# Kernel optimization log

Measured on AMD Instinct MI355X. Metric: run time of the kernel, lower is better.

Reference implementation:

```python
import jax, jax.numpy as jnp
import numpy as np

EMBED_DIM = 256
MIN_SCALE = 0.5
BASE = 100.0
NDIM = 3
EPS = 1e-5


def basis_norm(psi, w):
    # w: [B, N] float weights; reduce over token dim (-2)
    norm_sq = jnp.sum(w[..., None] * (psi * psi), axis=-2, keepdims=True)
    return psi / jnp.sqrt(norm_sq + EPS)


def rotary(f, coords, lift):
    # lift: [D//2, 3]; phase: [B, N, D//2]
    phase = coords @ lift.T
    c, s = jnp.cos(phase), jnp.sin(phase)
    f1, f2 = jnp.split(f, 2, axis=-1)
    return jnp.concatenate([f1 * c - f2 * s, f1 * s + f2 * c], axis=-1)


def setup_inputs() -> dict:
    key = jax.random.key(0)
    ks = jax.random.split(key, 12)
    B, N, D = 4, 8192, EMBED_DIM
    phi = jax.random.normal(ks[0], (B, N, D), dtype=jnp.float32)
    coords = jax.random.normal(ks[1], (B, N, NDIM), dtype=jnp.float32)
    weights = jax.random.uniform(ks[2], (B, N), dtype=jnp.float32)
    scale = 1.0 / np.sqrt(D)
    Wq = jax.random.normal(ks[3], (D, D), dtype=jnp.float32) * scale
    bq = jnp.zeros((D,), dtype=jnp.float32)
    Wk = jax.random.normal(ks[4], (D, D), dtype=jnp.float32) * scale
    bk = jax.random.normal(ks[5], (D,), dtype=jnp.float32) * 0.01
    Wv = jax.random.normal(ks[6], (D, D), dtype=jnp.float32) * scale
    bv = jax.random.normal(ks[7], (D,), dtype=jnp.float32) * 0.01
    Wo = jax.random.normal(ks[8], (D, D), dtype=jnp.float32) * scale
    bo = jnp.zeros((D,), dtype=jnp.float32)
    # rotary lift init: k_norms * random unit vecs
    half = D // 2
    scales = BASE ** (-2.0 * np.arange(half) / D)
    k_norms = (2.0 * np.pi / MIN_SCALE) * scales  # [half]
    u = np.asarray(jax.random.normal(ks[9], (half, NDIM)))
    u = u / np.linalg.norm(u, axis=-1, keepdims=True)
    lift = jnp.asarray(k_norms[:, None] * u, dtype=jnp.float32)  # [half, 3]
    return {"phi": phi, "coords": coords, "weights": weights,
            "Wq": Wq, "bq": bq, "Wk": Wk, "bk": bk, "Wv": Wv, "bv": bv,
            "Wo": Wo, "bo": bo, "lift": lift}


def reference(phi, coords, weights, Wq, bq, Wk, bk, Wv, bv, Wo, bo, lift):
    q = phi @ Wq.T + bq
    k = basis_norm(phi @ Wk.T + bk, weights)
    v = basis_norm(phi @ Wv.T + bv, weights)
    q = rotary(q, coords, lift)
    k = rotary(k, coords, lift)
    k = k * weights[..., None]  # float-weights branch
    kv = jnp.einsum('bnd,bne->bde', k, v)   # [B, D, D]
    out = jnp.einsum('bnd,bde->bne', q, kv)  # [B, N, D]
    return out @ Wo.T + bo
```

## Files before the change

### kernel.cpp

```cpp
#include <hip/hip_runtime.h>
#include <hip/hip_bf16.h>
#include <stdint.h>

#define DEV __device__ __forceinline__

typedef short short8 __attribute__((ext_vector_type(8)));
typedef float floatx4 __attribute__((ext_vector_type(4)));

constexpr int D = 256;
constexpr int NTOK = 8192;
constexpr int MTOT = 4 * NTOK;

DEV void gl_lds16(const void* g, void* l) {
  __builtin_amdgcn_global_load_lds(
      (const __attribute__((address_space(1))) void*)g,
      (__attribute__((address_space(3))) void*)l, 16, 0, 0);
}

DEV float bflo(uint32_t u) { return __uint_as_float(u << 16); }
DEV float bfhi(uint32_t u) { return __uint_as_float(u & 0xffff0000u); }
DEV uint32_t packbf(float a, float b) {
  uint16_t xa = __builtin_bit_cast(uint16_t, __float2bfloat16(a));
  uint16_t xb = __builtin_bit_cast(uint16_t, __float2bfloat16(b));
  return (uint32_t)xa | ((uint32_t)xb << 16);
}

constexpr int PHI_E = MTOT * D;
constexpr int W_E = D * D;

__global__ __launch_bounds__(256) void convert(
    const float* __restrict__ phi, const float* __restrict__ Wq,
    const float* __restrict__ Wk, const float* __restrict__ Wv,
    const float* __restrict__ Wo,
    uint2* __restrict__ dst, float2* __restrict__ nszero) {
  if (blockIdx.x == 0) {
    const float2 z = {0.f, 0.f};
#pragma unroll
    for (int k = 0; k < 4; k++) nszero[k * 256 + threadIdx.x] = z;
  }
  const int idx4 = blockIdx.x * 256 + threadIdx.x;
  const int e0 = idx4 * 4;
  float4 v;
  if (e0 < PHI_E) {
    v = ((const float4*)phi)[idx4];
  } else {
    const int r = e0 - PHI_E;
    const int m = r >> 16;
    const int q = (r & 65535) >> 2;
    const float4* src = (m == 0) ? (const float4*)Wq : (m == 1) ? (const float4*)Wk
                      : (m == 2) ? (const float4*)Wv : (const float4*)Wo;
    v = src[q];
  }
  uint2 o;
  o.x = packbf(v.x, v.y);
  o.y = packbf(v.z, v.w);
  dst[idx4] = o;
}

__global__ __launch_bounds__(256, 4) void gemm_qkv(
    const __hip_bfloat16* __restrict__ phi,
    const __hip_bfloat16* __restrict__ W16,
    const float* __restrict__ bq, const float* __restrict__ bk, const float* __restrict__ bv,
    const float* __restrict__ coords, const float* __restrict__ wts,
    const float* __restrict__ lift,
    __hip_bfloat16* __restrict__ Qb, __hip_bfloat16* __restrict__ Kb,
    __hip_bfloat16* __restrict__ Vb, float* __restrict__ nsk, float* __restrict__ nsv) {
  __shared__ __align__(16) char As[8192];
  __shared__ __align__(16) char Bs[8192];
  const int t = threadIdx.x, lane = t & 63, wid = t >> 6;
  const int wm = (wid & 1) * 64;
  const int wn = (wid >> 1) * 32;
  const int l16 = lane & 15, q4 = lane >> 4;
  const int bid = blockIdx.x;
  const int g = (bid & 7) * 192 + (bid >> 3);
  const int sub = g % 6;
  const int mat = sub >> 1;
  const int nc0 = (sub & 1) * 64;
  const int m0 = (g / 6) * 128;
  const __hip_bfloat16* W = W16 + (size_t)mat * W_E;
  const float* bias = (mat == 0) ? bq : (mat == 1) ? bk : bv;
  __hip_bfloat16* Out = (mat == 0) ? Qb : (mat == 1) ? Kb : Vb;

  floatx4 acc[4][4] = {};

  const int srow = wid * 16 + (lane >> 2);
  const int skoff = (lane & 3) * 8;
  const __hip_bfloat16* gA = phi + (size_t)(m0 + srow) * D + skoff;
  const __hip_bfloat16* gB = W + (size_t)(nc0 + srow) * D + skoff;
  char* lA = As + srow * 64 + skoff * 2;
  char* lB = Bs + srow * 64 + skoff * 2;

  for (int kt = 0; kt < 256; kt += 32) {
    gl_lds16(gA + kt, lA);
    gl_lds16(gA + kt + 64 * D, lA + 4096);
    gl_lds16(gB + kt, lB);
    gl_lds16(gB + kt + 128 * D, lB + 4096);
    __syncthreads();
    short8 af[4], bf4[4];
#pragma unroll
    for (int i = 0; i < 4; i++)
      af[i] = *(const short8*)(As + (wm + i * 16 + l16) * 64 + q4 * 16);
#pragma unroll
    for (int j = 0; j < 4; j++) {
      const int brow = (j >> 1) * 64 + wn + (j & 1) * 16 + l16;
      bf4[j] = *(const short8*)(Bs + brow * 64 + q4 * 16);
    }
#pragma unroll
    for (int i = 0; i < 4; i++)
#pragma unroll
      for (int j = 0; j < 4; j++)
        acc[i][j] = __builtin_amdgcn_mfma_f32_16x16x32_bf16(af[i], bf4[j], acc[i][j], 0, 0, 0);
    __syncthreads();
  }

  float bcol[4];
#pragma unroll
  for (int j = 0; j < 4; j++)
    bcol[j] = bias[nc0 + wn + (j & 1) * 16 + (j >> 1) * 128 + l16];

  if (mat == 0) {
    float lx[2], ly[2], lz[2];
#pragma unroll
    for (int jj = 0; jj < 2; jj++) {
      const int c = nc0 + wn + jj * 16 + l16;
      lx[jj] = lift[c * 3 + 0]; ly[jj] = lift[c * 3 + 1]; lz[jj] = lift[c * 3 + 2];
    }
#pragma unroll
    for (int i = 0; i < 4; i++) {
#pragma unroll
      for (int r = 0; r < 4; r++) {
        const int row = m0 + wm + i * 16 + q4 * 4 + r;
        const float cx = coords[row * 3 + 0];
        const float cy = coords[row * 3 + 1];
        const float cz = coords[row * 3 + 2];
#pragma unroll
        for (int jj = 0; jj < 2; jj++) {
          const int c = nc0 + wn + jj * 16 + l16;
          const float p = cx * lx[jj] + cy * ly[jj] + cz * lz[jj];
          float s, cs;
          __sincosf(p, &s, &cs);
          const float f1 = acc[i][jj][r] + bcol[jj];
          const float f2 = acc[i][jj + 2][r] + bcol[jj + 2];
          Out[(size_t)row * D + c]       = __float2bfloat16(f1 * cs - f2 * s);
          Out[(size_t)row * D + c + 128] = __float2bfloat16(f1 * s + f2 * cs);
        }
      }
    }
  } else {
    const int b = m0 >> 13;
    float* ns = (mat == 1) ? nsk : nsv;
    float colsum[4] = {};
#pragma unroll
    for (int i = 0; i < 4; i++) {
#pragma unroll
      for (int r = 0; r < 4; r++) {
        const int row = m0 + wm + i * 16 + q4 * 4 + r;
        const float w = wts[row];
#pragma unroll
        for (int j = 0; j < 4; j++) {
          const int col = nc0 + wn + (j & 1) * 16 + (j >> 1) * 128 + l16;
          const float psi = acc[i][j][r] + bcol[j];
          Out[(size_t)row * D + col] = __float2bfloat16(psi);
          colsum[j] += w * psi * psi;
        }
      }
    }
#pragma unroll
    for (int j = 0; j < 4; j++) {
      float s = colsum[j];
      s += __shfl_xor(s, 16);
      s += __shfl_xor(s, 32);
      if (q4 == 0) {
        const int col = nc0 + wn + (j & 1) * 16 + (j >> 1) * 128 + l16;
        atomicAdd(&ns[b * D + col], s);
      }
    }
  }
}

__global__ __launch_bounds__(256) void kpoint(
    __hip_bfloat16* __restrict__ Kb, const float* __restrict__ coords,
    const float* __restrict__ wts, const float* __restrict__ lift,
    const float* __restrict__ nsk) {
  const int t = threadIdx.x;
  const int j = t & 63, rloc = t >> 6;
  const int r0 = blockIdx.x * 32;
  const int b = r0 >> 13;
  const int j0 = 2 * j, j1 = 2 * j + 1;
  const float lx0 = lift[j0 * 3 + 0], ly0 = lift[j0 * 3 + 1], lz0 = lift[j0 * 3 + 2];
  const float lx1 = lift[j1 * 3 + 0], ly1 = lift[j1 * 3 + 1], lz1 = lift[j1 * 3 + 2];
  const int nb = b * D;
  const float ik0 = rsqrtf(nsk[nb + j0] + 1e-5f);
  const float ik1 = rsqrtf(nsk[nb + j1] + 1e-5f);
  const float ik2 = rsqrtf(nsk[nb + 128 + j0] + 1e-5f);
  const float ik3 = rsqrtf(nsk[nb + 128 + j1] + 1e-5f);
  uint32_t* K32 = (uint32_t*)Kb;
#pragma unroll
  for (int it = 0; it < 8; it++) {
    const size_t row = (size_t)r0 + it * 4 + rloc;
    const float cx = coords[row * 3 + 0];
    const float cy = coords[row * 3 + 1];
    const float cz = coords[row * 3 + 2];
    const float p0 = cx * lx0 + cy * ly0 + cz * lz0;
    const float p1 = cx * lx1 + cy * ly1 + cz * lz1;
    float s0, c0, s1, c1;
    __sincosf(p0, &s0, &c0);
    __sincosf(p1, &s1, &c1);
    const float w = wts[row];
    const size_t base = row * 128;
    const uint32_t klo = K32[base + j], khi = K32[base + 64 + j];
    const float k1a = bflo(klo) * ik0, k1b = bfhi(klo) * ik1;
    const float k2a = bflo(khi) * ik2, k2b = bfhi(khi) * ik3;
    K32[base + j]      = packbf((k1a * c0 - k2a * s0) * w, (k1b * c1 - k2b * s1) * w);
    K32[base + 64 + j] = packbf((k1a * s0 + k2a * c0) * w, (k1b * s1 + k2b * c1) * w);
  }
}

__global__ __launch_bounds__(256, 2) void gemm_tn(
    const __hip_bfloat16* __restrict__ Kwb, const __hip_bfloat16* __restrict__ Vb,
    __hip_bfloat16* __restrict__ part) {
  __shared__ __align__(16) char Asm[128 * 80];
  __shared__ __align__(16) char Bsm[128 * 80];
  const int t = threadIdx.x, lane = t & 63, wid = t >> 6;
  const int wm = (wid & 1) * 64, wn = (wid >> 1) * 64;
  const int l16 = lane & 15, q4 = lane >> 4;
  const int bid = blockIdx.x;
  const int g = (bid & 7) * 64 + (bid >> 3);
  const int ed = g & 3, rest = g >> 2;
  const int chunk = rest & 31, b = rest >> 5;
  const int d0 = (ed >> 1) * 128, e0 = (ed & 1) * 128;
  const uint32_t* A32 = (const uint32_t*)Kwb;
  const uint32_t* B32 = (const uint32_t*)Vb;
  const int s_np = (((t & 3) | ((t >> 6) << 2)) ^ ((t >> 4) & 3));
  const int s_e2lo = (t >> 2) & 15;
  floatx4 acc[4][4] = {};
  for (int nt = 0; nt < 256; nt += 32) {
    const int nbase = chunk * 256 + nt;
    const size_t tokbase = ((size_t)b * NTOK + nbase + 2 * s_np) * 128;
#pragma unroll
    for (int r = 0; r < 4; r++) {
      const int e2 = s_e2lo + r * 16;
      {
        const uint32_t a0 = A32[tokbase + (d0 >> 1) + e2];
        const uint32_t a1 = A32[tokbase + 128 + (d0 >> 1) + e2];
        *(uint32_t*)(Asm + (2 * e2) * 80 + 4 * s_np)     = (a0 & 0xffffu) | (a1 << 16);
        *(uint32_t*)(Asm + (2 * e2 + 1) * 80 + 4 * s_np) = (a0 >> 16) | (a1 & 0xffff0000u);
      }
      {
        const uint32_t b0 = B32[tokbase + (e0 >> 1) + e2];
        const uint32_t b1 = B32[tokbase + 128 + (e0 >> 1) + e2];
        *(uint32_t*)(Bsm + (2 * e2) * 80 + 4 * s_np)     = (b0 & 0xffffu) | (b1 << 16);
        *(uint32_t*)(Bsm + (2 * e2 + 1) * 80 + 4 * s_np) = (b0 >> 16) | (b1 & 0xffff0000u);
      }
    }
    __syncthreads();
    short8 af[4], bf8[4];
#pragma unroll
    for (int i = 0; i < 4; i++) {
      af[i]  = *(const short8*)(Asm + (wm + i * 16 + l16) * 80 + q4 * 16);
      bf8[i] = *(const short8*)(Bsm + (wn + i * 16 + l16) * 80 + q4 * 16);
    }
#pragma unroll
    for (int i = 0; i < 4; i++)
#pragma unroll
      for (int j = 0; j < 4; j++)
        acc[i][j] = __builtin_amdgcn_mfma_f32_16x16x32_bf16(af[i], bf8[j], acc[i][j], 0, 0, 0);
    __syncthreads();
  }
  __hip_bfloat16* pt = part + (((size_t)(chunk * 4 + b)) << 16);
#pragma unroll
  for (int i = 0; i < 4; i++) {
#pragma unroll
    for (int r = 0; r < 4; r++) {
      const int rg = d0 + wm + i * 16 + q4 * 4 + r;
#pragma unroll
      for (int j = 0; j < 4; j++) {
        const int cg = e0 + wn + j * 16 + l16;
        pt[rg * 256 + cg] = __float2bfloat16(acc[i][j][r]);
      }
    }
  }
}

__global__ __launch_bounds__(256) void reduce_kvt(const uint32_t* __restrict__ part,
                                                  uint32_t* __restrict__ Ps,
                                                  const float* __restrict__ nsv) {
  const int flat2 = blockIdx.x * 256 + threadIdx.x;
  const int b = flat2 >> 15;
  const int off = flat2 & 32767;
  const int es = (off & 127) * 2;
  float sx = 0, sy = 0;
#pragma unroll
  for (int c = 0; c < 32; c++) {
    const uint32_t u = part[(((size_t)(c * 4 + b)) << 15) + off];
    sx += bflo(u); sy += bfhi(u);
  }
  const float iv0 = rsqrtf(nsv[b * D + es] + 1e-5f);
  const float iv1 = rsqrtf(nsv[b * D + es + 1] + 1e-5f);
  Ps[flat2] = packbf(sx * iv0, sy * iv1);
}

__global__ __launch_bounds__(256, 4) void gemm_mt(
    const __hip_bfloat16* __restrict__ Wo16, const __hip_bfloat16* __restrict__ Ps,
    __hip_bfloat16* __restrict__ MT) {
  __shared__ __align__(16) char As[8192];
  __shared__ __align__(16) char Bs[8192];
  const int t = threadIdx.x, lane = t & 63, wid = t >> 6;
  const int wm = (wid & 1) * 64, wn = (wid >> 1) * 64;
  const int l16 = lane & 15, q4 = lane >> 4;
  const int m0 = blockIdx.x * 128, n0 = blockIdx.y * 128, b = blockIdx.z;
  const __hip_bfloat16* Bm = Ps + ((size_t)b << 16);
  floatx4 acc[4][4] = {};
  const int srow = wid * 16 + (lane >> 2);
  const int skoff = (lane & 3) * 8;
  const __hip_bfloat16* gA = Wo16 + (size_t)(m0 + srow) * D + skoff;
  const __hip_bfloat16* gB = Bm + (size_t)(n0 + srow) * D + skoff;
  char* lA = As + srow * 64 + skoff * 2;
  char* lB = Bs + srow * 64 + skoff * 2;
  for (int kt = 0; kt < 256; kt += 32) {
    gl_lds16(gA + kt, lA);
    gl_lds16(gA + kt + 64 * D, lA + 4096);
    gl_lds16(gB + kt, lB);
    gl_lds16(gB + kt + 64 * D, lB + 4096);
    __syncthreads();
    short8 af[4], bf8[4];
#pragma unroll
    for (int i = 0; i < 4; i++) {
      af[i]  = *(const short8*)(As + (wm + i * 16 + l16) * 64 + q4 * 16);
      bf8[i] = *(const short8*)(Bs + (wn + i * 16 + l16) * 64 + q4 * 16);
    }
#pragma unroll
    for (int i = 0; i < 4; i++)
#pragma unroll
      for (int j = 0; j < 4; j++)
        acc[i][j] = __builtin_amdgcn_mfma_f32_16x16x32_bf16(af[i], bf8[j], acc[i][j], 0, 0, 0);
    __syncthreads();
  }
  __hip_bfloat16* Ob = MT + ((size_t)b << 16);
#pragma unroll
  for (int j = 0; j < 4; j++) {
    const int colg = n0 + wn + j * 16 + l16;
#pragma unroll
    for (int i = 0; i < 4; i++) {
      const int rowg = m0 + wm + i * 16 + q4 * 4;
#pragma unroll
      for (int r = 0; r < 4; r++)
        Ob[(size_t)(rowg + r) * D + colg] = __float2bfloat16(acc[i][j][r]);
    }
  }
}

__global__ __launch_bounds__(256, 4) void gemm_out(
    const __hip_bfloat16* __restrict__ A, const __hip_bfloat16* __restrict__ Pm,
    const float* __restrict__ bo, float* __restrict__ Og) {
  __shared__ __align__(16) char As[8192];
  __shared__ __align__(16) char Bs[8192];
  const int t = threadIdx.x, lane = t & 63, wid = t >> 6;
  const int wm = (wid & 1) * 64, wn = (wid >> 1) * 64;
  const int l16 = lane & 15, q4 = lane >> 4;
  const int m0 = blockIdx.x * 128, n0 = blockIdx.y * 128;
  const int b = m0 >> 13;
  const __hip_bfloat16* W = Pm + ((size_t)b << 16);
  floatx4 acc[4][4] = {};
  const int srow = wid * 16 + (lane >> 2);
  const int skoff = (lane & 3) * 8;
  const __hip_bfloat16* gA = A + (size_t)(m0 + srow) * D + skoff;
  const __hip_bfloat16* gB = W + (size_t)(n0 + srow) * D + skoff;
  char* lA = As + srow * 64 + skoff * 2;
  char* lB = Bs + srow * 64 + skoff * 2;
  for (int kt = 0; kt < 256; kt += 32) {
    gl_lds16(gA + kt, lA);
    gl_lds16(gA + kt + 64 * D, lA + 4096);
    gl_lds16(gB + kt, lB);
    gl_lds16(gB + kt + 64 * D, lB + 4096);
    __syncthreads();
    short8 af[4], bf8[4];
#pragma unroll
    for (int i = 0; i < 4; i++) {
      af[i]  = *(const short8*)(As + (wm + i * 16 + l16) * 64 + q4 * 16);
      bf8[i] = *(const short8*)(Bs + (wn + i * 16 + l16) * 64 + q4 * 16);
    }
#pragma unroll
    for (int i = 0; i < 4; i++)
#pragma unroll
      for (int j = 0; j < 4; j++)
        acc[i][j] = __builtin_amdgcn_mfma_f32_16x16x32_bf16(af[i], bf8[j], acc[i][j], 0, 0, 0);
    __syncthreads();
  }
#pragma unroll
  for (int j = 0; j < 4; j++) {
    const int colg = n0 + wn + j * 16 + l16;
    const float bb = bo[colg];
#pragma unroll
    for (int i = 0; i < 4; i++) {
      const int rowg = m0 + wm + i * 16 + q4 * 4;
#pragma unroll
      for (int r = 0; r < 4; r++)
        Og[(size_t)(rowg + r) * D + colg] = acc[i][j][r] + bb;
    }
  }
}

extern "C" void kernel_launch(void* const* d_in, const int* in_sizes, int n_in,
                              void* d_out, int out_size, void* d_ws, size_t ws_size,
                              hipStream_t stream) {
  const float* phi    = (const float*)d_in[0];
  const float* coords = (const float*)d_in[1];
  const float* wts    = (const float*)d_in[2];
  const float* bq     = (const float*)d_in[4];
  const float* bk     = (const float*)d_in[6];
  const float* bv     = (const float*)d_in[8];
  const float* Wo     = (const float*)d_in[9];
  const float* bo     = (const float*)d_in[10];
  const float* lift   = (const float*)d_in[11];

  char* ws = (char*)d_ws;
  __hip_bfloat16* phi16 = (__hip_bfloat16*)ws;
  __hip_bfloat16* W16   = (__hip_bfloat16*)(ws + 16777216);
  const size_t QOFF = 17301504;
  const size_t SZ = (size_t)MTOT * D * 2;
  __hip_bfloat16* Qb = (__hip_bfloat16*)(ws + QOFF);
  __hip_bfloat16* Kb = (__hip_bfloat16*)(ws + QOFF + SZ);
  __hip_bfloat16* Vb = (__hip_bfloat16*)(ws + QOFF + 2 * SZ);
  const size_t NOFF = QOFF + 3 * SZ;
  float* nsk = (float*)(ws + NOFF);
  float* nsv = (float*)(ws + NOFF + 4096);
  __hip_bfloat16* part = (__hip_bfloat16*)(ws + NOFF + 8192);
  __hip_bfloat16* Ps   = (__hip_bfloat16*)(ws + NOFF + 8192 + 16777216);
  __hip_bfloat16* MT   = (__hip_bfloat16*)(ws + NOFF + 8192 + 16777216 + 524288);

  convert<<<8448, 256, 0, stream>>>(phi, (const float*)d_in[3], (const float*)d_in[5],
                                    (const float*)d_in[7], Wo,
                                    (uint2*)ws, (float2*)(ws + NOFF));
  gemm_qkv<<<1536, 256, 0, stream>>>(phi16, W16, bq, bk, bv, coords, wts, lift,
                                     Qb, Kb, Vb, nsk, nsv);
  kpoint<<<1024, 256, 0, stream>>>(Kb, coords, wts, lift, nsk);
  gemm_tn<<<512, 256, 0, stream>>>(Kb, Vb, part);
  reduce_kvt<<<512, 256, 0, stream>>>((const uint32_t*)part, (uint32_t*)Ps, nsv);
  gemm_mt<<<dim3(2, 2, 4), 256, 0, stream>>>(W16 + 3 * W_E, Ps, MT);
  gemm_out<<<dim3(256, 2), 256, 0, stream>>>(Qb, MT, bo, (float*)d_out);
}
```

Measured before the change: 177.0 us.

## Fuse K normalization, rotary and weighting into the K^T V gemm loader

Removes the separate kpoint pass that read, rotated and rewrote K in global memory. gemm_tn's A-tile loader now loads each K element together with its rotary partner half and the token coords and weights. It computes sin/cos on the fly and applies the norm, rotation and weight before packing into LDS. This saves a full read+write of K at the cost of extra loads and sincos work inside the GEMM, which is repeated for each output tile that reads the same K. The launch bounds of gemm_mt and gemm_out are also relaxed from 4 to 2 blocks per CU.

```diff
diff --git a/kernel.cpp b/kernel.cpp
--- a/kernel.cpp
+++ b/kernel.cpp
@@ -178,47 +178,11 @@
   }
 }
 
-__global__ __launch_bounds__(256) void kpoint(
-    __hip_bfloat16* __restrict__ Kb, const float* __restrict__ coords,
+__global__ __launch_bounds__(256, 2) void gemm_tn(
+    const __hip_bfloat16* __restrict__ Kwb, const __hip_bfloat16* __restrict__ Vb,
+    __hip_bfloat16* __restrict__ part, const float* __restrict__ coords,
     const float* __restrict__ wts, const float* __restrict__ lift,
     const float* __restrict__ nsk) {
-  const int t = threadIdx.x;
-  const int j = t & 63, rloc = t >> 6;
-  const int r0 = blockIdx.x * 32;
-  const int b = r0 >> 13;
-  const int j0 = 2 * j, j1 = 2 * j + 1;
-  const float lx0 = lift[j0 * 3 + 0], ly0 = lift[j0 * 3 + 1], lz0 = lift[j0 * 3 + 2];
-  const float lx1 = lift[j1 * 3 + 0], ly1 = lift[j1 * 3 + 1], lz1 = lift[j1 * 3 + 2];
-  const int nb = b * D;
-  const float ik0 = rsqrtf(nsk[nb + j0] + 1e-5f);
-  const float ik1 = rsqrtf(nsk[nb + j1] + 1e-5f);
-  const float ik2 = rsqrtf(nsk[nb + 128 + j0] + 1e-5f);
-  const float ik3 = rsqrtf(nsk[nb + 128 + j1] + 1e-5f);
-  uint32_t* K32 = (uint32_t*)Kb;
-#pragma unroll
-  for (int it = 0; it < 8; it++) {
-    const size_t row = (size_t)r0 + it * 4 + rloc;
-    const float cx = coords[row * 3 + 0];
-    const float cy = coords[row * 3 + 1];
-    const float cz = coords[row * 3 + 2];
-    const float p0 = cx * lx0 + cy * ly0 + cz * lz0;
-    const float p1 = cx * lx1 + cy * ly1 + cz * lz1;
-    float s0, c0, s1, c1;
-    __sincosf(p0, &s0, &c0);
-    __sincosf(p1, &s1, &c1);
-    const float w = wts[row];
-    const size_t base = row * 128;
-    const uint32_t klo = K32[base + j], khi = K32[base + 64 + j];
-    const float k1a = bflo(klo) * ik0, k1b = bfhi(klo) * ik1;
-    const float k2a = bflo(khi) * ik2, k2b = bfhi(khi) * ik3;
-    K32[base + j]      = packbf((k1a * c0 - k2a * s0) * w, (k1b * c1 - k2b * s1) * w);
-    K32[base + 64 + j] = packbf((k1a * s0 + k2a * c0) * w, (k1b * s1 + k2b * c1) * w);
-  }
-}
-
-__global__ __launch_bounds__(256, 2) void gemm_tn(
-    const __hip_bfloat16* __restrict__ Kwb, const __hip_bfloat16* __restrict__ Vb,
-    __hip_bfloat16* __restrict__ part) {
   __shared__ __align__(16) char Asm[128 * 80];
   __shared__ __align__(16) char Bsm[128 * 80];
   const int t = threadIdx.x, lane = t & 63, wid = t >> 6;
@@ -233,18 +197,54 @@
   const uint32_t* B32 = (const uint32_t*)Vb;
   const int s_np = (((t & 3) | ((t >> 6) << 2)) ^ ((t >> 4) & 3));
   const int s_e2lo = (t >> 2) & 15;
+  float ikA[4], ikB[4], ikC[4], ikD[4];
+  float lxa[4], lya[4], lza[4], lxb[4], lyb[4], lzb[4];
+#pragma unroll
+  for (int r = 0; r < 4; r++) {
+    const int cl = 2 * (s_e2lo + r * 16);
+    ikA[r] = rsqrtf(nsk[b * D + cl] + 1e-5f);
+    ikB[r] = rsqrtf(nsk[b * D + cl + 1] + 1e-5f);
+    ikC[r] = rsqrtf(nsk[b * D + cl + 128] + 1e-5f);
+    ikD[r] = rsqrtf(nsk[b * D + cl + 129] + 1e-5f);
+    lxa[r] = lift[cl * 3 + 0]; lya[r] = lift[cl * 3 + 1]; lza[r] = lift[cl * 3 + 2];
+    lxb[r] = lift[cl * 3 + 3]; lyb[r] = lift[cl * 3 + 4]; lzb[r] = lift[cl * 3 + 5];
+  }
   floatx4 acc[4][4] = {};
   for (int nt = 0; nt < 256; nt += 32) {
     const int nbase = chunk * 256 + nt;
-    const size_t tokbase = ((size_t)b * NTOK + nbase + 2 * s_np) * 128;
+    const size_t gt0 = (size_t)b * NTOK + nbase + 2 * s_np;
+    const size_t tokbase = gt0 * 128;
+    const float cx0 = coords[gt0 * 3 + 0], cy0 = coords[gt0 * 3 + 1], cz0 = coords[gt0 * 3 + 2];
+    const float cx1 = coords[gt0 * 3 + 3], cy1 = coords[gt0 * 3 + 4], cz1 = coords[gt0 * 3 + 5];
+    const float w0 = wts[gt0], w1 = wts[gt0 + 1];
 #pragma unroll
     for (int r = 0; r < 4; r++) {
       const int e2 = s_e2lo + r * 16;
+      const int dwA = (d0 >> 1) + e2;
       {
-        const uint32_t a0 = A32[tokbase + (d0 >> 1) + e2];
-        const uint32_t a1 = A32[tokbase + 128 + (d0 >> 1) + e2];
-        *(uint32_t*)(Asm + (2 * e2) * 80 + 4 * s_np)     = (a0 & 0xffffu) | (a1 << 16);
-        *(uint32_t*)(Asm + (2 * e2 + 1) * 80 + 4 * s_np) = (a0 >> 16) | (a1 & 0xffff0000u);
+        const uint32_t a0 = A32[tokbase + dwA];
+        const uint32_t a1 = A32[tokbase + 128 + dwA];
+        const uint32_t p0 = A32[tokbase + (dwA ^ 64)];
+        const uint32_t p1 = A32[tokbase + 128 + (dwA ^ 64)];
+        float s00, c00, s01, c01, s10, c10, s11, c11;
+        __sincosf(cx0 * lxa[r] + cy0 * lya[r] + cz0 * lza[r], &s00, &c00);
+        __sincosf(cx0 * lxb[r] + cy0 * lyb[r] + cz0 * lzb[r], &s01, &c01);
+        __sincosf(cx1 * lxa[r] + cy1 * lya[r] + cz1 * lza[r], &s10, &c10);
+        __sincosf(cx1 * lxb[r] + cy1 * lyb[r] + cz1 * lzb[r], &s11, &c11);
+        float oT0a, oT0b, oT1a, oT1b;
+        if (d0 == 0) {
+          oT0a = (bflo(a0) * ikA[r] * c00 - bflo(p0) * ikC[r] * s00) * w0;
+          oT0b = (bfhi(a0) * ikB[r] * c01 - bfhi(p0) * ikD[r] * s01) * w0;
+          oT1a = (bflo(a1) * ikA[r] * c10 - bflo(p1) * ikC[r] * s10) * w1;
+          oT1b = (bfhi(a1) * ikB[r] * c11 - bfhi(p1) * ikD[r] * s11) * w1;
+        } else {
+          oT0a = (bflo(p0) * ikA[r] * s00 + bflo(a0) * ikC[r] * c00) * w0;
+          oT0b = (bfhi(p0) * ikB[r] * s01 + bfhi(a0) * ikD[r] * c01) * w0;
+          oT1a = (bflo(p1) * ikA[r] * s10 + bflo(a1) * ikC[r] * c10) * w1;
+          oT1b = (bfhi(p1) * ikB[r] * s11 + bfhi(a1) * ikD[r] * c11) * w1;
+        }
+        *(uint32_t*)(Asm + (2 * e2) * 80 + 4 * s_np)     = packbf(oT0a, oT1a);
+        *(uint32_t*)(Asm + (2 * e2 + 1) * 80 + 4 * s_np) = packbf(oT0b, oT1b);
       }
       {
         const uint32_t b0 = B32[tokbase + (e0 >> 1) + e2];
@@ -300,7 +300,7 @@
   Ps[flat2] = packbf(sx * iv0, sy * iv1);
 }
 
-__global__ __launch_bounds__(256, 4) void gemm_mt(
+__global__ __launch_bounds__(256, 2) void gemm_mt(
     const __hip_bfloat16* __restrict__ Wo16, const __hip_bfloat16* __restrict__ Ps,
     __hip_bfloat16* __restrict__ MT) {
   __shared__ __align__(16) char As[8192];
@@ -350,7 +350,7 @@
   }
 }
 
-__global__ __launch_bounds__(256, 4) void gemm_out(
+__global__ __launch_bounds__(256, 2) void gemm_out(
     const __hip_bfloat16* __restrict__ A, const __hip_bfloat16* __restrict__ Pm,
     const float* __restrict__ bo, float* __restrict__ Og) {
   __shared__ __align__(16) char As[8192];
@@ -434,8 +434,7 @@
                                     (uint2*)ws, (float2*)(ws + NOFF));
   gemm_qkv<<<1536, 256, 0, stream>>>(phi16, W16, bq, bk, bv, coords, wts, lift,
                                      Qb, Kb, Vb, nsk, nsv);
-  kpoint<<<1024, 256, 0, stream>>>(Kb, coords, wts, lift, nsk);
-  gemm_tn<<<512, 256, 0, stream>>>(Kb, Vb, part);
+  gemm_tn<<<512, 256, 0, stream>>>(Kb, Vb, part, coords, wts, lift, nsk);
   reduce_kvt<<<512, 256, 0, stream>>>((const uint32_t*)part, (uint32_t*)Ps, nsv);
   gemm_mt<<<dim3(2, 2, 4), 256, 0, stream>>>(W16 + 3 * W_E, Ps, MT);
   gemm_out<<<dim3(256, 2), 256, 0, stream>>>(Qb, MT, bo, (float*)d_out);
```

Measured after the change: 174.4 us. No clear change (-1.5%).
